# Optimization experiments

Hardware: AMD Instinct MI355X
Metric: run time of the kernel (lower is better)

Reference implementation:

```python
import jax, jax.numpy as jnp
import numpy as np

B, L, DM, H, DH = 4, 2048, 768, 12, 64

def setup_inputs() -> dict:
    key = jax.random.key(0)
    ks = jax.random.split(key, 5)
    s = 1.0 / np.sqrt(DM)
    return {
        "x": jax.random.normal(ks[0], (B, L, DM), dtype=jnp.float32),
        "Wq": jax.random.normal(ks[1], (DM, H, DH), dtype=jnp.float32) * s,
        "bq": jnp.zeros((H, DH), dtype=jnp.float32),
        "Wk": jax.random.normal(ks[2], (DM, H, DH), dtype=jnp.float32) * s,
        "bk": jnp.zeros((H, DH), dtype=jnp.float32),
        "Wv": jax.random.normal(ks[3], (DM, H, DH), dtype=jnp.float32) * s,
        "bv": jnp.zeros((H, DH), dtype=jnp.float32),
        "Wd": jax.random.normal(ks[4], (H, DH, DM), dtype=jnp.float32) * (1.0 / np.sqrt(H * DH)),
        "bd": jnp.zeros((DM,), dtype=jnp.float32),
    }

def reference(x, Wq, bq, Wk, bk, Wv, bv, Wd, bd):
    # QKV projections: [B,L,DM] x [DM,H,DH] -> [B,L,H,DH]
    q = jnp.einsum('blm,mhd->blhd', x, Wq) + bq
    k = jnp.einsum('blm,mhd->blhd', x, Wk) + bk
    v = jnp.einsum('blm,mhd->blhd', x, Wv) + bv
    # NOTE: original module has NO 1/sqrt(dhead) scaling
    a = jnp.einsum('blhd,bLhd->bhlL', q, k)      # [B,H,L,L] scores
    a = jax.nn.softmax(a, axis=-1)
    prefinal = jnp.einsum('bhlL,bLhd->blhd', a, v)
    out = jnp.einsum('blhd,hdm->blm', prefinal, Wd) + bd
    return out
```

## Files before the change

### kernel.cpp

```cpp
#include <hip/hip_runtime.h>
#include <math.h>

constexpr int B  = 4;
constexpr int L  = 2048;
constexpr int DM = 768;
constexpr int H  = 12;
constexpr int DH = 64;
constexpr int M  = B * L;
constexpr float LOG2E = 1.4426950408889634f;

typedef __attribute__((ext_vector_type(8)))  _Float16       f16x8;
typedef __attribute__((ext_vector_type(8)))  short          s16x8;
typedef __attribute__((ext_vector_type(4)))  unsigned short u16x4;
typedef __attribute__((ext_vector_type(8)))  unsigned short u16x8;
typedef __attribute__((ext_vector_type(4)))  unsigned int   u32x4;
typedef __attribute__((ext_vector_type(16))) float          f32x16;
typedef __attribute__((ext_vector_type(4)))  float          f32x4;
typedef unsigned short ushort_t;
typedef unsigned int   uint_t;

#define MFMA16(a, b, c) __builtin_amdgcn_mfma_f32_32x32x16_f16((a), (b), (c), 0, 0, 0)

#if __has_builtin(__builtin_amdgcn_exp2f)
#define EXP2(x) __builtin_amdgcn_exp2f(x)
#else
#define EXP2(x) exp2f(x)
#endif

__device__ __forceinline__ ushort_t h_bits(_Float16 h) {
    return __builtin_bit_cast(ushort_t, h);
}
__device__ __forceinline__ uint_t pkrtz(float a, float b) {
    return __builtin_bit_cast(uint_t, __builtin_amdgcn_cvt_pkrtz(a, b));
}
__device__ __forceinline__ void plswap(uint_t& x, uint_t& y) {
    asm volatile("v_permlane32_swap_b32 %0, %1" : "+v"(x), "+v"(y));
}

__global__ __launch_bounds__(256) void cast_x(
    const float* __restrict__ x, ushort_t* __restrict__ xh, int n)
{
    const int i = (blockIdx.x * 256 + threadIdx.x) * 4;
    if (i >= n) return;
    const float4 v = *reinterpret_cast<const float4*>(&x[i]);
    u16x4 hh;
    hh[0] = h_bits((_Float16)v.x); hh[1] = h_bits((_Float16)v.y);
    hh[2] = h_bits((_Float16)v.z); hh[3] = h_bits((_Float16)v.w);
    *reinterpret_cast<u16x4*>(&xh[i]) = hh;
}

__global__ __launch_bounds__(256) void wtransAll(
    const float* __restrict__ W0, const float* __restrict__ W1,
    const float* __restrict__ W2, const float* __restrict__ W3,
    ushort_t* __restrict__ T0, ushort_t* __restrict__ T1,
    ushort_t* __restrict__ T2, ushort_t* __restrict__ T3)
{
    __shared__ ushort_t Tls[64][72];
    const int t = threadIdx.x;
    const int k0 = blockIdx.x * 64, n0 = blockIdx.y * 64, wsel = blockIdx.z;
    const float* W = wsel == 0 ? W0 : wsel == 1 ? W1 : wsel == 2 ? W2 : W3;
    ushort_t*    T = wsel == 0 ? T0 : wsel == 1 ? T1 : wsel == 2 ? T2 : T3;

    #pragma unroll
    for (int it = 0; it < 4; ++it) {
        const int idx = it * 256 + t;
        const int r = idx >> 4, c = (idx & 15) * 4;
        const float4 v = *reinterpret_cast<const float4*>(
            &W[(size_t)(k0 + r) * 768 + n0 + c]);
        Tls[c + 0][r] = h_bits((_Float16)v.x);
        Tls[c + 1][r] = h_bits((_Float16)v.y);
        Tls[c + 2][r] = h_bits((_Float16)v.z);
        Tls[c + 3][r] = h_bits((_Float16)v.w);
    }
    __syncthreads();
    #pragma unroll
    for (int it = 0; it < 4; ++it) {
        const int idx = it * 256 + t;
        const int r = idx >> 4, c = (idx & 15) * 4;
        *reinterpret_cast<u16x4*>(&T[(size_t)(n0 + r) * 768 + k0 + c]) =
            *reinterpret_cast<const u16x4*>(&Tls[r][c]);
    }
}

template<int EPI, int QS>
__global__ __launch_bounds__(256) void gemm2(
    const ushort_t* __restrict__ Ah, const ushort_t* __restrict__ Wh,
    const float* __restrict__ bias, void* __restrict__ out0)
{
    constexpr int KD = 768;
    __shared__ __align__(16) ushort_t Ahs[128][40];
    __shared__ __align__(16) ushort_t Whs[96][40];
    __shared__ __align__(16) ushort_t Ots[EPI == 1 ? 96 : 1][EPI == 1 ? 136 : 8];

    const int t = threadIdx.x, lane = t & 63, w = t >> 6;
    const int l31 = lane & 31, l5 = lane >> 5;
    const int m0 = blockIdx.x * 128, n0 = blockIdx.y * 96;
    const int arow = t >> 1, acol = (t & 1) * 16;
    const int wrow = t >> 1, wcol = (t & 1) * 16;

    f32x16 acc[3] = {};
    s16x8 rA0, rA1, rW0, rW1;

    auto LOAD = [&](int k0) {
        const size_t ab = (size_t)(m0 + arow) * KD + k0 + acol;
        rA0 = *reinterpret_cast<const s16x8*>(&Ah[ab]);
        rA1 = *reinterpret_cast<const s16x8*>(&Ah[ab + 8]);
        if (t < 192) {
            const size_t wb = (size_t)(n0 + wrow) * KD + k0 + wcol;
            rW0 = *reinterpret_cast<const s16x8*>(&Wh[wb]);
            rW1 = *reinterpret_cast<const s16x8*>(&Wh[wb + 8]);
        }
    };
    auto STORE = [&]() {
        *reinterpret_cast<s16x8*>(&Ahs[arow][acol])     = rA0;
        *reinterpret_cast<s16x8*>(&Ahs[arow][acol + 8]) = rA1;
        if (t < 192) {
            *reinterpret_cast<s16x8*>(&Whs[wrow][wcol])     = rW0;
            *reinterpret_cast<s16x8*>(&Whs[wrow][wcol + 8]) = rW1;
        }
    };

    LOAD(0); STORE();
    __syncthreads();

    for (int k0 = 0; k0 < KD; k0 += 32) {
        if (k0 + 32 < KD) LOAD(k0 + 32);
        #pragma unroll
        for (int ks = 0; ks < 2; ++ks) {
            const int koff = ks * 16 + l5 * 8;
            const f16x8 af = *reinterpret_cast<const f16x8*>(&Ahs[w * 32 + l31][koff]);
            #pragma unroll
            for (int nt = 0; nt < 3; ++nt) {
                const f16x8 wf = *reinterpret_cast<const f16x8*>(&Whs[nt * 32 + l31][koff]);
                acc[nt] = MFMA16(af, wf, acc[nt]);
            }
        }
        __syncthreads();
        if (k0 + 32 < KD) STORE();
        __syncthreads();
    }

    if constexpr (EPI == 1) {
        #pragma unroll
        for (int nt = 0; nt < 3; ++nt) {
            const float bb = bias[n0 + nt * 32 + l31];
            #pragma unroll
            for (int reg = 0; reg < 16; ++reg) {
                const int rowl = (reg & 3) + 8 * (reg >> 2) + 4 * l5;
                Ots[nt * 32 + l31][w * 32 + rowl] =
                    h_bits((_Float16)(acc[nt][reg] + bb));
            }
        }
        __syncthreads();
        ushort_t* vt = (ushort_t*)out0;
        const int bq = m0 >> 11, lq = m0 & 2047;
        #pragma unroll
        for (int it = 0; it < 6; ++it) {
            const int idx = it * 256 + t;
            const int r = idx >> 4, c = (idx & 15) * 8;
            const int n = n0 + r, hh = n >> 6, dh = n & 63;
            *reinterpret_cast<u16x8*>(
                &vt[((((size_t)bq * H + hh) * DH + dh) << 11) + lq + c]) =
                *reinterpret_cast<const u16x8*>(&Ots[r][c]);
        }
    } else {
        #pragma unroll
        for (int nt = 0; nt < 3; ++nt) {
            const int n = n0 + nt * 32 + l31;
            const float bb = bias[n];
            #pragma unroll
            for (int reg = 0; reg < 16; ++reg) {
                const int rowl = (reg & 3) + 8 * (reg >> 2) + 4 * l5;
                const int m = m0 + w * 32 + rowl;
                float v = acc[nt][reg] + bb;
                if constexpr (QS) v *= LOG2E;
                if constexpr (EPI == 2) {
                    ((float*)out0)[(size_t)m * 768 + n] = v;
                } else {
                    ((ushort_t*)out0)[(size_t)m * 768 + n] = h_bits((_Float16)v);
                }
            }
        }
    }
}

__global__ __launch_bounds__(256) void attn2(
    const ushort_t* __restrict__ qh, const ushort_t* __restrict__ kh,
    const ushort_t* __restrict__ vt, ushort_t* __restrict__ pf)
{
    __shared__ __align__(16) ushort_t Khs[64][72];
    __shared__ __align__(16) ushort_t Vts[64][72];
    __shared__ __align__(16) float scale_s[4][32];
    __shared__ __align__(16) float l_s[4][32];

    const int t = threadIdx.x, lane = t & 63, w = t >> 6;
    const int l31 = lane & 31, l5 = lane >> 5;
    const int qt = blockIdx.x, h = blockIdx.y, b = blockIdx.z;

    const int qrow = qt * 128 + w * 32 + l31;
    const size_t qb = ((size_t)(b * L + qrow)) * 768 + h * 64;
    f16x8 qfh[4];
    #pragma unroll
    for (int ks = 0; ks < 4; ++ks)
        qfh[ks] = *reinterpret_cast<const f16x8*>(&qh[qb + ks * 16 + l5 * 8]);

    f32x16 o[2] = {};
    float m_run = -3.0e38f, l_run = 0.0f;
    const int sr = t >> 3, scc = (t & 7) * 8;
    s16x8 rK0, rK1, rV0, rV1;

    auto LOADT = [&](int kt) {
        const size_t kg = ((size_t)(b * L + kt * 64 + sr)) * 768 + h * 64 + scc;
        rK0 = *reinterpret_cast<const s16x8*>(&kh[kg]);
        rK1 = *reinterpret_cast<const s16x8*>(&kh[kg + (size_t)32 * 768]);
        const size_t vg = (((size_t)b * H + h) * DH + sr) * (size_t)L + kt * 64 + scc;
        rV0 = *reinterpret_cast<const s16x8*>(&vt[vg]);
        rV1 = *reinterpret_cast<const s16x8*>(&vt[vg + (size_t)32 * L]);
    };
    auto STORET = [&]() {
        *reinterpret_cast<s16x8*>(&Khs[sr][scc])      = rK0;
        *reinterpret_cast<s16x8*>(&Khs[sr + 32][scc]) = rK1;
        *reinterpret_cast<s16x8*>(&Vts[sr][scc])      = rV0;
        *reinterpret_cast<s16x8*>(&Vts[sr + 32][scc]) = rV1;
    };

    LOADT(0); STORET();
    __syncthreads();

    for (int kt = 0; kt < L / 64; ++kt) {
        if (kt + 1 < L / 64) LOADT(kt + 1);

        f32x16 st[2] = {};
        #pragma unroll
        for (int mt = 0; mt < 2; ++mt) {
            #pragma unroll
            for (int ks = 0; ks < 4; ++ks) {
                const f16x8 kf = *reinterpret_cast<const f16x8*>(
                    &Khs[mt * 32 + l31][ks * 16 + l5 * 8]);
                st[mt] = MFMA16(kf, qfh[ks], st[mt]);
            }
        }

        float pmax = -3.0e38f;
        #pragma unroll
        for (int mt = 0; mt < 2; ++mt)
            #pragma unroll
            for (int e = 0; e < 16; ++e) pmax = fmaxf(pmax, st[mt][e]);
        pmax = fmaxf(pmax, __shfl_xor(pmax, 32));

        if (!__all(pmax - m_run <= 12.0f)) {
            const float mnew = fmaxf(m_run, pmax);
            const float sc = EXP2(m_run - mnew);
            m_run = mnew;
            l_run *= sc;
            scale_s[w][l31] = sc;
            #pragma unroll
            for (int rg = 0; rg < 4; ++rg) {
                const f32x4 sc4 =
                    *reinterpret_cast<const f32x4*>(&scale_s[w][8 * rg + 4 * l5]);
                #pragma unroll
                for (int j = 0; j < 4; ++j) {
                    o[0][rg * 4 + j] *= sc4[j];
                    o[1][rg * 4 + j] *= sc4[j];
                }
            }
        }

        float sum = 0.0f;
        #pragma unroll
        for (int mt = 0; mt < 2; ++mt)
            #pragma unroll
            for (int e = 0; e < 16; ++e) {
                const float p = EXP2(st[mt][e] - m_run);
                st[mt][e] = p;
                sum += p;
            }
        sum += __shfl_xor(sum, 32);
        l_run += sum;

        f16x8 pa[4];
        #pragma unroll
        for (int mt = 0; mt < 2; ++mt) {
            #pragma unroll
            for (int hf = 0; hf < 2; ++hf) {
                uint_t a0 = pkrtz(st[mt][8 * hf + 0], st[mt][8 * hf + 1]);
                uint_t a1 = pkrtz(st[mt][8 * hf + 2], st[mt][8 * hf + 3]);
                uint_t b0 = pkrtz(st[mt][8 * hf + 4], st[mt][8 * hf + 5]);
                uint_t b1 = pkrtz(st[mt][8 * hf + 6], st[mt][8 * hf + 7]);
                plswap(a0, b0);
                plswap(a1, b1);
                u32x4 pk4; pk4[0] = a0; pk4[1] = a1; pk4[2] = b0; pk4[3] = b1;
                pa[mt * 2 + hf] = __builtin_bit_cast(f16x8, pk4);
            }
        }

        #pragma unroll
        for (int ks = 0; ks < 4; ++ks) {
            const int koff = ks * 16 + l5 * 8;
            #pragma unroll
            for (int dt = 0; dt < 2; ++dt) {
                const f16x8 vb =
                    *reinterpret_cast<const f16x8*>(&Vts[dt * 32 + l31][koff]);
                o[dt] = MFMA16(pa[ks], vb, o[dt]);
            }
        }

        __syncthreads();
        if (kt + 1 < L / 64) STORET();
        __syncthreads();
    }

    l_s[w][l31] = l_run;
    const size_t ob = ((size_t)(b * L + qt * 128 + w * 32)) * 768 + h * 64;
    #pragma unroll
    for (int rg = 0; rg < 4; ++rg) {
        const f32x4 lv = *reinterpret_cast<const f32x4*>(&l_s[w][8 * rg + 4 * l5]);
        #pragma unroll
        for (int j = 0; j < 4; ++j) {
            const float inv = 1.0f / lv[j];
            const int rowl = j + 8 * rg + 4 * l5;
            #pragma unroll
            for (int dt = 0; dt < 2; ++dt) {
                pf[ob + (size_t)rowl * 768 + dt * 32 + l31] =
                    h_bits((_Float16)(o[dt][rg * 4 + j] * inv));
            }
        }
    }
}

extern "C" void kernel_launch(void* const* d_in, const int* in_sizes, int n_in,
                              void* d_out, int out_size, void* d_ws, size_t ws_size,
                              hipStream_t stream)
{
    const float* x  = (const float*)d_in[0];
    const float* Wq = (const float*)d_in[1];
    const float* bq = (const float*)d_in[2];
    const float* Wk = (const float*)d_in[3];
    const float* bk = (const float*)d_in[4];
    const float* Wv = (const float*)d_in[5];
    const float* bv = (const float*)d_in[6];
    const float* Wd = (const float*)d_in[7];
    const float* bd = (const float*)d_in[8];
    float* out = (float*)d_out;

    constexpr size_t S  = (size_t)M * 768;
    constexpr size_t WS = (size_t)768 * 768;
    ushort_t* p = (ushort_t*)d_ws;
    ushort_t* xh  = p; p += S;
    ushort_t* qhb = p; p += S;
    ushort_t* khb = p; p += S;
    ushort_t* vtb = p; p += S;
    ushort_t* WqT = p; p += WS;
    ushort_t* WkT = p; p += WS;
    ushort_t* WvT = p; p += WS;
    ushort_t* WdT = p; p += WS;
    ushort_t* pfb = xh;

    cast_x<<<dim3((int)(S / 1024)), dim3(256), 0, stream>>>(x, xh, (int)S);
    wtransAll<<<dim3(12, 12, 4), dim3(256), 0, stream>>>(
        Wq, Wk, Wv, Wd, WqT, WkT, WvT, WdT);

    const dim3 gg(M / 128, DM / 96);
    const dim3 blk(256);

    gemm2<3, 1><<<gg, blk, 0, stream>>>(xh, WqT, bq, qhb);
    gemm2<3, 0><<<gg, blk, 0, stream>>>(xh, WkT, bk, khb);
    gemm2<1, 0><<<gg, blk, 0, stream>>>(xh, WvT, bv, vtb);

    attn2<<<dim3(L / 128, H, B), blk, 0, stream>>>(qhb, khb, vtb, pfb);

    gemm2<2, 0><<<gg, blk, 0, stream>>>(pfb, WdT, bd, out);
}
```

Baseline: 252.4 us.

## Merge QKV projections into one launch and halve attention block size

Merges the three Q/K/V projection GEMMs into a single kernel launch that selects its weights by grid y index. The V transpose epilogue now uses a smaller shared-memory tile aliased over the GEMM staging buffers. The attention kernel moves to 128-thread blocks of 64 query rows, doubling the grid to improve occupancy and load balance, at the cost of loading each K/V tile twice as often. It also replaces the cross-half shuffles with permlane32 swaps and splits the softmax sums into independent accumulators to shorten dependency chains.

```diff
diff --git a/kernel.cpp b/kernel.cpp
--- a/kernel.cpp
+++ b/kernel.cpp
@@ -35,6 +35,20 @@
 }
 __device__ __forceinline__ void plswap(uint_t& x, uint_t& y) {
     asm volatile("v_permlane32_swap_b32 %0, %1" : "+v"(x), "+v"(y));
+}
+__device__ __forceinline__ float half_max(float v) {
+    uint_t a = __builtin_bit_cast(uint_t, v);
+    uint_t b;
+    asm("v_mov_b32 %0, %1" : "=&v"(b) : "v"(a));
+    plswap(a, b);
+    return fmaxf(__builtin_bit_cast(float, a), __builtin_bit_cast(float, b));
+}
+__device__ __forceinline__ float half_sum(float v) {
+    uint_t a = __builtin_bit_cast(uint_t, v);
+    uint_t b;
+    asm("v_mov_b32 %0, %1" : "=&v"(b) : "v"(a));
+    plswap(a, b);
+    return __builtin_bit_cast(float, a) + __builtin_bit_cast(float, b);
 }
 
 __global__ __launch_bounds__(256) void cast_x(
@@ -82,15 +96,118 @@
     }
 }
 
-template<int EPI, int QS>
-__global__ __launch_bounds__(256) void gemm2(
+__global__ __launch_bounds__(256) void qkvproj(
+    const ushort_t* __restrict__ xh,
+    const ushort_t* __restrict__ WqT, const ushort_t* __restrict__ WkT,
+    const ushort_t* __restrict__ WvT,
+    const float* __restrict__ bq, const float* __restrict__ bk,
+    const float* __restrict__ bv,
+    ushort_t* __restrict__ qhb, ushort_t* __restrict__ khb,
+    ushort_t* __restrict__ vtb)
+{
+    constexpr int KD = 768;
+    __shared__ __align__(16) char pool[17920];
+    ushort_t (*Ahs)[40] = (ushort_t(*)[40])pool;
+    ushort_t (*Whs)[40] = (ushort_t(*)[40])(pool + 10240);
+    ushort_t (*Ots)[136] = (ushort_t(*)[136])pool;
+
+    const int t = threadIdx.x, lane = t & 63, w = t >> 6;
+    const int l31 = lane & 31, l5 = lane >> 5;
+    const int which = blockIdx.y >> 3;
+    const int m0 = blockIdx.x * 128, n0 = (blockIdx.y & 7) * 96;
+    const ushort_t* Wh = which == 0 ? WqT : which == 1 ? WkT : WvT;
+    const float* bias  = which == 0 ? bq  : which == 1 ? bk  : bv;
+    const int arow = t >> 1, acol = (t & 1) * 16;
+    const int wrow = t >> 1, wcol = (t & 1) * 16;
+
+    f32x16 acc[3] = {};
+    s16x8 rA0, rA1, rW0, rW1;
+
+    auto LOAD = [&](int k0) {
+        const size_t ab = (size_t)(m0 + arow) * KD + k0 + acol;
+        rA0 = *reinterpret_cast<const s16x8*>(&xh[ab]);
+        rA1 = *reinterpret_cast<const s16x8*>(&xh[ab + 8]);
+        if (t < 192) {
+            const size_t wb = (size_t)(n0 + wrow) * KD + k0 + wcol;
+            rW0 = *reinterpret_cast<const s16x8*>(&Wh[wb]);
+            rW1 = *reinterpret_cast<const s16x8*>(&Wh[wb + 8]);
+        }
+    };
+    auto STORE = [&]() {
+        *reinterpret_cast<s16x8*>(&Ahs[arow][acol])     = rA0;
+        *reinterpret_cast<s16x8*>(&Ahs[arow][acol + 8]) = rA1;
+        if (t < 192) {
+            *reinterpret_cast<s16x8*>(&Whs[wrow][wcol])     = rW0;
+            *reinterpret_cast<s16x8*>(&Whs[wrow][wcol + 8]) = rW1;
+        }
+    };
+
+    LOAD(0); STORE();
+    __syncthreads();
+
+    for (int k0 = 0; k0 < KD; k0 += 32) {
+        if (k0 + 32 < KD) LOAD(k0 + 32);
+        #pragma unroll
+        for (int ks = 0; ks < 2; ++ks) {
+            const int koff = ks * 16 + l5 * 8;
+            const f16x8 af = *reinterpret_cast<const f16x8*>(&Ahs[w * 32 + l31][koff]);
+            #pragma unroll
+            for (int nt = 0; nt < 3; ++nt) {
+                const f16x8 wf = *reinterpret_cast<const f16x8*>(&Whs[nt * 32 + l31][koff]);
+                acc[nt] = MFMA16(af, wf, acc[nt]);
+            }
+        }
+        __syncthreads();
+        if (k0 + 32 < KD) STORE();
+        __syncthreads();
+    }
+
+    if (which == 2) {
+        const int bq_ = m0 >> 11, lq = m0 & 2047;
+        #pragma unroll
+        for (int nt = 0; nt < 3; ++nt) {
+            const float bb = bias[n0 + nt * 32 + l31];
+            __syncthreads();
+            #pragma unroll
+            for (int reg = 0; reg < 16; ++reg) {
+                const int rowl = (reg & 3) + 8 * (reg >> 2) + 4 * l5;
+                Ots[l31][w * 32 + rowl] = h_bits((_Float16)(acc[nt][reg] + bb));
+            }
+            __syncthreads();
+            #pragma unroll
+            for (int it = 0; it < 2; ++it) {
+                const int idx = it * 256 + t;
+                const int r = idx >> 4, c = (idx & 15) * 8;
+                const int n = n0 + nt * 32 + r, hh = n >> 6, dh = n & 63;
+                *reinterpret_cast<u16x8*>(
+                    &vtb[((((size_t)bq_ * H + hh) * DH + dh) << 11) + lq + c]) =
+                    *reinterpret_cast<const u16x8*>(&Ots[r][c]);
+            }
+        }
+    } else {
+        ushort_t* out = which == 0 ? qhb : khb;
+        const float qs = which == 0 ? LOG2E : 1.0f;
+        #pragma unroll
+        for (int nt = 0; nt < 3; ++nt) {
+            const int n = n0 + nt * 32 + l31;
+            const float bb = bias[n];
+            #pragma unroll
+            for (int reg = 0; reg < 16; ++reg) {
+                const int rowl = (reg & 3) + 8 * (reg >> 2) + 4 * l5;
+                const int m = m0 + w * 32 + rowl;
+                out[(size_t)m * 768 + n] = h_bits((_Float16)((acc[nt][reg] + bb) * qs));
+            }
+        }
+    }
+}
+
+__global__ __launch_bounds__(256) void gemm_out(
     const ushort_t* __restrict__ Ah, const ushort_t* __restrict__ Wh,
-    const float* __restrict__ bias, void* __restrict__ out0)
+    const float* __restrict__ bias, float* __restrict__ out)
 {
     constexpr int KD = 768;
     __shared__ __align__(16) ushort_t Ahs[128][40];
     __shared__ __align__(16) ushort_t Whs[96][40];
-    __shared__ __align__(16) ushort_t Ots[EPI == 1 ? 96 : 1][EPI == 1 ? 136 : 8];
 
     const int t = threadIdx.x, lane = t & 63, w = t >> 6;
     const int l31 = lane & 31, l5 = lane >> 5;
@@ -140,64 +257,33 @@
         __syncthreads();
     }
 
-    if constexpr (EPI == 1) {
-        #pragma unroll
-        for (int nt = 0; nt < 3; ++nt) {
-            const float bb = bias[n0 + nt * 32 + l31];
-            #pragma unroll
-            for (int reg = 0; reg < 16; ++reg) {
-                const int rowl = (reg & 3) + 8 * (reg >> 2) + 4 * l5;
-                Ots[nt * 32 + l31][w * 32 + rowl] =
-                    h_bits((_Float16)(acc[nt][reg] + bb));
-            }
-        }
-        __syncthreads();
-        ushort_t* vt = (ushort_t*)out0;
-        const int bq = m0 >> 11, lq = m0 & 2047;
-        #pragma unroll
-        for (int it = 0; it < 6; ++it) {
-            const int idx = it * 256 + t;
-            const int r = idx >> 4, c = (idx & 15) * 8;
-            const int n = n0 + r, hh = n >> 6, dh = n & 63;
-            *reinterpret_cast<u16x8*>(
-                &vt[((((size_t)bq * H + hh) * DH + dh) << 11) + lq + c]) =
-                *reinterpret_cast<const u16x8*>(&Ots[r][c]);
-        }
-    } else {
-        #pragma unroll
-        for (int nt = 0; nt < 3; ++nt) {
-            const int n = n0 + nt * 32 + l31;
-            const float bb = bias[n];
-            #pragma unroll
-            for (int reg = 0; reg < 16; ++reg) {
-                const int rowl = (reg & 3) + 8 * (reg >> 2) + 4 * l5;
-                const int m = m0 + w * 32 + rowl;
-                float v = acc[nt][reg] + bb;
-                if constexpr (QS) v *= LOG2E;
-                if constexpr (EPI == 2) {
-                    ((float*)out0)[(size_t)m * 768 + n] = v;
-                } else {
-                    ((ushort_t*)out0)[(size_t)m * 768 + n] = h_bits((_Float16)v);
-                }
-            }
-        }
-    }
-}
-
-__global__ __launch_bounds__(256) void attn2(
+    #pragma unroll
+    for (int nt = 0; nt < 3; ++nt) {
+        const int n = n0 + nt * 32 + l31;
+        const float bb = bias[n];
+        #pragma unroll
+        for (int reg = 0; reg < 16; ++reg) {
+            const int rowl = (reg & 3) + 8 * (reg >> 2) + 4 * l5;
+            const int m = m0 + w * 32 + rowl;
+            out[(size_t)m * 768 + n] = acc[nt][reg] + bb;
+        }
+    }
+}
+
+__global__ __launch_bounds__(128) void attn2(
     const ushort_t* __restrict__ qh, const ushort_t* __restrict__ kh,
     const ushort_t* __restrict__ vt, ushort_t* __restrict__ pf)
 {
     __shared__ __align__(16) ushort_t Khs[64][72];
     __shared__ __align__(16) ushort_t Vts[64][72];
-    __shared__ __align__(16) float scale_s[4][32];
-    __shared__ __align__(16) float l_s[4][32];
+    __shared__ __align__(16) float scale_s[2][32];
+    __shared__ __align__(16) float l_s[2][32];
 
     const int t = threadIdx.x, lane = t & 63, w = t >> 6;
     const int l31 = lane & 31, l5 = lane >> 5;
     const int qt = blockIdx.x, h = blockIdx.y, b = blockIdx.z;
 
-    const int qrow = qt * 128 + w * 32 + l31;
+    const int qrow = qt * 64 + w * 32 + l31;
     const size_t qb = ((size_t)(b * L + qrow)) * 768 + h * 64;
     f16x8 qfh[4];
     #pragma unroll
@@ -207,21 +293,29 @@
     f32x16 o[2] = {};
     float m_run = -3.0e38f, l_run = 0.0f;
     const int sr = t >> 3, scc = (t & 7) * 8;
-    s16x8 rK0, rK1, rV0, rV1;
+    s16x8 rK0, rK1, rK2, rK3, rV0, rV1, rV2, rV3;
 
     auto LOADT = [&](int kt) {
         const size_t kg = ((size_t)(b * L + kt * 64 + sr)) * 768 + h * 64 + scc;
         rK0 = *reinterpret_cast<const s16x8*>(&kh[kg]);
-        rK1 = *reinterpret_cast<const s16x8*>(&kh[kg + (size_t)32 * 768]);
+        rK1 = *reinterpret_cast<const s16x8*>(&kh[kg + (size_t)16 * 768]);
+        rK2 = *reinterpret_cast<const s16x8*>(&kh[kg + (size_t)32 * 768]);
+        rK3 = *reinterpret_cast<const s16x8*>(&kh[kg + (size_t)48 * 768]);
         const size_t vg = (((size_t)b * H + h) * DH + sr) * (size_t)L + kt * 64 + scc;
         rV0 = *reinterpret_cast<const s16x8*>(&vt[vg]);
-        rV1 = *reinterpret_cast<const s16x8*>(&vt[vg + (size_t)32 * L]);
+        rV1 = *reinterpret_cast<const s16x8*>(&vt[vg + (size_t)16 * L]);
+        rV2 = *reinterpret_cast<const s16x8*>(&vt[vg + (size_t)32 * L]);
+        rV3 = *reinterpret_cast<const s16x8*>(&vt[vg + (size_t)48 * L]);
     };
     auto STORET = [&]() {
         *reinterpret_cast<s16x8*>(&Khs[sr][scc])      = rK0;
-        *reinterpret_cast<s16x8*>(&Khs[sr + 32][scc]) = rK1;
+        *reinterpret_cast<s16x8*>(&Khs[sr + 16][scc]) = rK1;
+        *reinterpret_cast<s16x8*>(&Khs[sr + 32][scc]) = rK2;
+        *reinterpret_cast<s16x8*>(&Khs[sr + 48][scc]) = rK3;
         *reinterpret_cast<s16x8*>(&Vts[sr][scc])      = rV0;
-        *reinterpret_cast<s16x8*>(&Vts[sr + 32][scc]) = rV1;
+        *reinterpret_cast<s16x8*>(&Vts[sr + 16][scc]) = rV1;
+        *reinterpret_cast<s16x8*>(&Vts[sr + 32][scc]) = rV2;
+        *reinterpret_cast<s16x8*>(&Vts[sr + 48][scc]) = rV3;
     };
 
     LOADT(0); STORET();
@@ -241,12 +335,15 @@
             }
         }
 
-        float pmax = -3.0e38f;
-        #pragma unroll
-        for (int mt = 0; mt < 2; ++mt)
-            #pragma unroll
-            for (int e = 0; e < 16; ++e) pmax = fmaxf(pmax, st[mt][e]);
-        pmax = fmaxf(pmax, __shfl_xor(pmax, 32));
+        float mx[8];
+        #pragma unroll
+        for (int i = 0; i < 8; ++i)
+            mx[i] = fmaxf(fmaxf(st[0][i], st[0][i + 8]),
+                          fmaxf(st[1][i], st[1][i + 8]));
+        mx[0] = fmaxf(mx[0], mx[4]); mx[1] = fmaxf(mx[1], mx[5]);
+        mx[2] = fmaxf(mx[2], mx[6]); mx[3] = fmaxf(mx[3], mx[7]);
+        mx[0] = fmaxf(fmaxf(mx[0], mx[2]), fmaxf(mx[1], mx[3]));
+        const float pmax = half_max(mx[0]);
 
         if (!__all(pmax - m_run <= 12.0f)) {
             const float mnew = fmaxf(m_run, pmax);
@@ -266,17 +363,20 @@
             }
         }
 
-        float sum = 0.0f;
+        float s0 = 0.f, s1 = 0.f, s2 = 0.f, s3 = 0.f;
         #pragma unroll
         for (int mt = 0; mt < 2; ++mt)
             #pragma unroll
-            for (int e = 0; e < 16; ++e) {
-                const float p = EXP2(st[mt][e] - m_run);
-                st[mt][e] = p;
-                sum += p;
-            }
-        sum += __shfl_xor(sum, 32);
-        l_run += sum;
+            for (int e = 0; e < 16; e += 4) {
+                const float p0 = EXP2(st[mt][e + 0] - m_run);
+                const float p1 = EXP2(st[mt][e + 1] - m_run);
+                const float p2 = EXP2(st[mt][e + 2] - m_run);
+                const float p3 = EXP2(st[mt][e + 3] - m_run);
+                st[mt][e + 0] = p0; st[mt][e + 1] = p1;
+                st[mt][e + 2] = p2; st[mt][e + 3] = p3;
+                s0 += p0; s1 += p1; s2 += p2; s3 += p3;
+            }
+        l_run += half_sum((s0 + s1) + (s2 + s3));
 
         f16x8 pa[4];
         #pragma unroll
@@ -311,7 +411,7 @@
     }
 
     l_s[w][l31] = l_run;
-    const size_t ob = ((size_t)(b * L + qt * 128 + w * 32)) * 768 + h * 64;
+    const size_t ob = ((size_t)(b * L + qt * 64 + w * 32)) * 768 + h * 64;
     #pragma unroll
     for (int rg = 0; rg < 4; ++rg) {
         const f32x4 lv = *reinterpret_cast<const f32x4*>(&l_s[w][8 * rg + 4 * l5]);
@@ -360,14 +460,10 @@
     wtransAll<<<dim3(12, 12, 4), dim3(256), 0, stream>>>(
         Wq, Wk, Wv, Wd, WqT, WkT, WvT, WdT);
 
-    const dim3 gg(M / 128, DM / 96);
-    const dim3 blk(256);
-
-    gemm2<3, 1><<<gg, blk, 0, stream>>>(xh, WqT, bq, qhb);
-    gemm2<3, 0><<<gg, blk, 0, stream>>>(xh, WkT, bk, khb);
-    gemm2<1, 0><<<gg, blk, 0, stream>>>(xh, WvT, bv, vtb);
-
-    attn2<<<dim3(L / 128, H, B), blk, 0, stream>>>(qhb, khb, vtb, pfb);
-
-    gemm2<2, 0><<<gg, blk, 0, stream>>>(pfb, WdT, bd, out);
-}
+    qkvproj<<<dim3(M / 128, 24), dim3(256), 0, stream>>>(
+        xh, WqT, WkT, WvT, bq, bk, bv, qhb, khb, vtb);
+
+    attn2<<<dim3(L / 64, H, B), dim3(128), 0, stream>>>(qhb, khb, vtb, pfb);
+
+    gemm_out<<<dim3(M / 128, DM / 96), dim3(256), 0, stream>>>(pfb, WdT, bd, out);
+}
```

After: 268.4 us. 6.4% more time.
